# Optimization experiments

Hardware: AMD Instinct MI355X
Metric: run time of the kernel (lower is better)

The kernel has to match this reference:

```python
import jax, jax.numpy as jnp
import numpy as np

N_NODES = 50000
N_EDGES = 800000
IN_CH = 128
OUT_CH = 64
HEADS = 8


def setup_inputs() -> dict:
    key = jax.random.key(0)
    k1, k2, k3, k4 = jax.random.split(key, 4)
    x = jax.random.normal(k1, (N_NODES, IN_CH), dtype=jnp.float32)
    edge_index = jax.random.randint(k2, (2, N_EDGES), 0, N_NODES, dtype=jnp.int32)
    # xavier-uniform-ish scale
    W = jax.random.normal(k3, (IN_CH, OUT_CH), dtype=jnp.float32) * (1.0 / np.sqrt(IN_CH))
    attn_weights = jax.random.normal(k4, (2 * OUT_CH, 1), dtype=jnp.float32) * (1.0 / np.sqrt(2 * OUT_CH))
    return {"x": x, "edge_index": edge_index, "W": W, "attn_weights": attn_weights}


def reference(x, edge_index, W, attn_weights):
    # h: [N, out]
    h = x @ W
    ei, ej = edge_index[0], edge_index[1]
    h_i = h[ei]                      # [E, out] gather by destination
    h_j = h[ej]                      # [E, out] gather by source
    edge_feat = jnp.concatenate([h_i, h_j], axis=-1)  # [E, 2*out]
    logits = jax.nn.leaky_relu(edge_feat @ attn_weights, negative_slope=0.2)  # [E, 1]
    # NOTE: original does softmax over dim=0 -> GLOBAL softmax over all edges
    alpha = jax.nn.softmax(logits, axis=0)  # [E, 1]
    # dropout p=0.6 is a no-op in eval mode (training=False)
    msg = h_j * alpha                # [E, out]
    h_head = jnp.zeros_like(h).at[ei].add(msg)  # scatter-add into destinations
    # All heads share W and attn_weights (see source loop), so with dropout off
    # every head is identical; concat == tile along feature dim.
    return jnp.tile(h_head, (1, HEADS))  # [N, out*heads]
```

## Files before the change

kernel.cpp:

```cpp
#include <hip/hip_runtime.h>

#define N_NODES 50000
#define N_EDGES 800000
#define IN_CH 128
#define OUT_CH 64
#define HEADS 8
#define ROW 512
#define NBLK_G 782
#define NBLK_A 782
#define NBIN 196
#define BINCAP 4608
#define MAXDEG 64
#define WS_STRIDE 136

typedef float f4 __attribute__((ext_vector_type(4)));
typedef short bf16x8 __attribute__((ext_vector_type(8)));

__device__ __forceinline__ float lrelu(float z) {
    return z > 0.0f ? z : 0.2f * z;
}

__device__ __forceinline__ unsigned f2b(float f) {
    unsigned u = __float_as_uint(f);
    return (u + 0x7FFFu + ((u >> 16) & 1u)) >> 16;
}

__global__ __launch_bounds__(256) void gemm_bin(const float* __restrict__ x,
                                                const float* __restrict__ W,
                                                const float* __restrict__ attn,
                                                const int4* __restrict__ ei4,
                                                const int4* __restrict__ ej4,
                                                unsigned short* __restrict__ hbuf,
                                                float* __restrict__ s,
                                                float* __restrict__ t,
                                                int* __restrict__ bin_count,
                                                unsigned* __restrict__ binned) {
    __shared__ unsigned short xs[64 * WS_STRIDE];
    __shared__ unsigned short wls[64 * WS_STRIDE];
    const int tid = threadIdx.x;
    const int bid = blockIdx.x;

    if (bid & 1) {
        unsigned* hist = (unsigned*)xs;
        unsigned* bse  = hist + NBIN;
        unsigned* cur  = bse + NBIN;
        if (tid < NBIN) { hist[tid] = 0u; cur[tid] = 0u; }
        __syncthreads();
        const int g = (bid >> 1) * 256 + tid;
        const bool act = g < N_EDGES / 4;
        int4 li = make_int4(0, 0, 0, 0), lj = make_int4(0, 0, 0, 0);
        if (act) {
            li = ei4[g];
            lj = ej4[g];
            atomicAdd(&hist[li.x >> 8], 1u);
            atomicAdd(&hist[li.y >> 8], 1u);
            atomicAdd(&hist[li.z >> 8], 1u);
            atomicAdd(&hist[li.w >> 8], 1u);
        }
        __syncthreads();
        if (tid < NBIN) {
            const unsigned c = hist[tid];
            bse[tid] = c ? (unsigned)atomicAdd(&bin_count[tid], (int)c) : 0u;
        }
        __syncthreads();
        if (act) {
            const unsigned p0 = bse[li.x >> 8] + atomicAdd(&cur[li.x >> 8], 1u);
            if (p0 < BINCAP) binned[(li.x >> 8) * BINCAP + p0] =
                ((unsigned)(li.x & 255) << 16) | (unsigned)lj.x;
            const unsigned p1 = bse[li.y >> 8] + atomicAdd(&cur[li.y >> 8], 1u);
            if (p1 < BINCAP) binned[(li.y >> 8) * BINCAP + p1] =
                ((unsigned)(li.y & 255) << 16) | (unsigned)lj.y;
            const unsigned p2 = bse[li.z >> 8] + atomicAdd(&cur[li.z >> 8], 1u);
            if (p2 < BINCAP) binned[(li.z >> 8) * BINCAP + p2] =
                ((unsigned)(li.z & 255) << 16) | (unsigned)lj.z;
            const unsigned p3 = bse[li.w >> 8] + atomicAdd(&cur[li.w >> 8], 1u);
            if (p3 < BINCAP) binned[(li.w >> 8) * BINCAP + p3] =
                ((unsigned)(li.w & 255) << 16) | (unsigned)lj.w;
        }
        return;
    }

    const int base = (bid >> 1) * 64;
    {
        const float4* W4 = (const float4*)W;
#pragma unroll
        for (int j = 0; j < 8; ++j) {
            const int idx = tid + j * 256;
            const int k = idx >> 4;
            const int c = (idx & 15) * 4;
            const float4 v = W4[idx];
            wls[(c + 0) * WS_STRIDE + k] = (unsigned short)f2b(v.x);
            wls[(c + 1) * WS_STRIDE + k] = (unsigned short)f2b(v.y);
            wls[(c + 2) * WS_STRIDE + k] = (unsigned short)f2b(v.z);
            wls[(c + 3) * WS_STRIDE + k] = (unsigned short)f2b(v.w);
        }
    }
    {
        const float4* x4 = (const float4*)x;
#pragma unroll
        for (int j = 0; j < 8; ++j) {
            const int idx = tid + j * 256;
            const int r = idx >> 5;
            const int kq = idx & 31;
            const int row = base + r;
            float4 v = make_float4(0.f, 0.f, 0.f, 0.f);
            if (row < N_NODES) v = x4[row * 32 + kq];
            ushort4 pb;
            pb.x = (unsigned short)f2b(v.x);
            pb.y = (unsigned short)f2b(v.y);
            pb.z = (unsigned short)f2b(v.z);
            pb.w = (unsigned short)f2b(v.w);
            *(ushort4*)&xs[r * WS_STRIDE + kq * 4] = pb;
        }
    }
    __syncthreads();
    const int w = tid >> 6, lane = tid & 63;
    const int m = lane & 15;
    const int kq = lane >> 4;
    bf16x8 afr[4];
#pragma unroll
    for (int kb = 0; kb < 4; ++kb)
        afr[kb] = *(const bf16x8*)&xs[(w * 16 + m) * WS_STRIDE + kb * 32 + kq * 8];
    float sacc[4] = {0.f, 0.f, 0.f, 0.f};
    float tacc[4] = {0.f, 0.f, 0.f, 0.f};
#pragma unroll
    for (int ct = 0; ct < 4; ++ct) {
        f4 acc = {0.f, 0.f, 0.f, 0.f};
#pragma unroll
        for (int kb = 0; kb < 4; ++kb) {
            const bf16x8 b = *(const bf16x8*)&wls[(ct * 16 + m) * WS_STRIDE + kb * 32 + kq * 8];
            acc = __builtin_amdgcn_mfma_f32_16x16x32_bf16(afr[kb], b, acc, 0, 0, 0);
        }
        const float a1 = attn[ct * 16 + m];
        const float a2 = attn[64 + ct * 16 + m];
#pragma unroll
        for (int r = 0; r < 4; ++r) {
            sacc[r] = fmaf(acc[r], a1, sacc[r]);
            tacc[r] = fmaf(acc[r], a2, tacc[r]);
            const int row = base + w * 16 + kq * 4 + r;
            if (row < N_NODES)
                hbuf[row * OUT_CH + ct * 16 + m] = (unsigned short)f2b(acc[r]);
        }
    }
#pragma unroll
    for (int off = 1; off < 16; off <<= 1) {
#pragma unroll
        for (int r = 0; r < 4; ++r) {
            sacc[r] += __shfl_xor(sacc[r], off, 64);
            tacc[r] += __shfl_xor(tacc[r], off, 64);
        }
    }
    if (m == 0) {
#pragma unroll
        for (int r = 0; r < 4; ++r) {
            const int row = base + w * 16 + kq * 4 + r;
            if (row < N_NODES) { s[row] = sacc[r]; t[row] = tacc[r]; }
        }
    }
}

__global__ __launch_bounds__(1024) void weight_pass(const unsigned* __restrict__ binned,
                                                    const int* __restrict__ bin_count,
                                                    const float* __restrict__ s,
                                                    const float* __restrict__ t,
                                                    unsigned* __restrict__ cv,
                                                    int* __restrict__ count,
                                                    float* __restrict__ Zsum) {
    __shared__ unsigned bkt[256 * MAXDEG];
    __shared__ unsigned cnt_l[256];
    __shared__ float s_l[256];
    __shared__ float red[16];
    const int tid = threadIdx.x;
    const int bin = blockIdx.x;
    if (tid < 256) {
        cnt_l[tid] = 0u;
        const int d = bin * 256 + tid;
        s_l[tid] = (d < N_NODES) ? s[d] : 0.0f;
    }
    __syncthreads();
    int n = bin_count[bin];
    if (n > BINCAP) n = BINCAP;
    float zs = 0.0f;
    for (int i = tid; i < n; i += 1024) {
        const unsigned e = binned[bin * BINCAP + i];
        const int dl = (int)((e >> 16) & 255u);
        const int src = (int)(e & 0xFFFFu);
        const float w = __expf(lrelu(s_l[dl] + t[src]));
        zs += w;
        const unsigned r = atomicAdd(&cnt_l[dl], 1u);
        if (r < MAXDEG) bkt[dl * MAXDEG + r] = (f2b(w) << 16) | (unsigned)src;
    }
    __syncthreads();
    {
        uint4* cv4 = (uint4*)(cv + bin * (256 * MAXDEG));
        const uint4* b4 = (const uint4*)bkt;
        for (int i = tid; i < 4096; i += 1024) cv4[i] = b4[i];
    }
    if (tid < 256) {
        const int d = bin * 256 + tid;
        if (d < N_NODES) count[d] = (int)cnt_l[tid];
    }
#pragma unroll
    for (int off = 32; off > 0; off >>= 1)
        zs += __shfl_down(zs, off, 64);
    if ((tid & 63) == 0) red[tid >> 6] = zs;
    __syncthreads();
    if (tid == 0) {
        float v = 0.0f;
#pragma unroll
        for (int k = 0; k < 16; ++k) v += red[k];
        atomicAdd(Zsum, v);
    }
}

__global__ __launch_bounds__(256) void gather_out(const int* __restrict__ count,
                                                  const unsigned* __restrict__ cv,
                                                  const float* __restrict__ Zsum,
                                                  const unsigned short* __restrict__ hbuf,
                                                  float* __restrict__ out) {
    const int n = blockIdx.x * 4 + (threadIdx.x >> 6);
    const int lane = threadIdx.x & 63;
    const int slot = lane >> 3;
    const int q = lane & 7;
    const float z = 1.0f / Zsum[0];
    int cnt = count[n];
    cnt = cnt < MAXDEG ? cnt : MAXDEG;
    const int base = n * MAXDEG;
    const uint4* h4 = (const uint4*)hbuf;
    f4 a0 = (f4)(0.0f);
    f4 a1 = (f4)(0.0f);
    unsigned pk = 0u;
    if (slot < cnt) pk = cv[base + slot];
    for (int i = 0; i < cnt; i += 8) {
        const int c = (int)(pk & 0xFFFFu);
        const float w = __uint_as_float(pk & 0xFFFF0000u);
        unsigned pk_n = 0u;
        const int ee = i + 8 + slot;
        if (ee < cnt) pk_n = cv[base + ee];
        const uint4 hv = h4[c * 8 + q];
        a0.x = fmaf(w, __uint_as_float(hv.x << 16),        a0.x);
        a0.y = fmaf(w, __uint_as_float(hv.x & 0xFFFF0000u), a0.y);
        a0.z = fmaf(w, __uint_as_float(hv.y << 16),        a0.z);
        a0.w = fmaf(w, __uint_as_float(hv.y & 0xFFFF0000u), a0.w);
        a1.x = fmaf(w, __uint_as_float(hv.z << 16),        a1.x);
        a1.y = fmaf(w, __uint_as_float(hv.z & 0xFFFF0000u), a1.y);
        a1.z = fmaf(w, __uint_as_float(hv.w << 16),        a1.z);
        a1.w = fmaf(w, __uint_as_float(hv.w & 0xFFFF0000u), a1.w);
        pk = pk_n;
    }
#pragma unroll
    for (int off = 8; off <= 32; off <<= 1) {
        a0.x += __shfl_xor(a0.x, off, 64);
        a0.y += __shfl_xor(a0.y, off, 64);
        a0.z += __shfl_xor(a0.z, off, 64);
        a0.w += __shfl_xor(a0.w, off, 64);
        a1.x += __shfl_xor(a1.x, off, 64);
        a1.y += __shfl_xor(a1.y, off, 64);
        a1.z += __shfl_xor(a1.z, off, 64);
        a1.w += __shfl_xor(a1.w, off, 64);
    }
    a0 *= z;
    a1 *= z;
    f4* out4 = (f4*)out;
    const int ob = n * 128 + slot * 16 + q * 2;
    __builtin_nontemporal_store(a0, out4 + ob);
    __builtin_nontemporal_store(a1, out4 + ob + 1);
}

extern "C" void kernel_launch(void* const* d_in, const int* in_sizes, int n_in,
                              void* d_out, int out_size, void* d_ws, size_t ws_size,
                              hipStream_t stream) {
    const float* x    = (const float*)d_in[0];
    const int*   eidx = (const int*)d_in[1];
    const float* W    = (const float*)d_in[2];
    const float* attn = (const float*)d_in[3];
    float* out = (float*)d_out;

    unsigned short* hbuf = (unsigned short*)d_ws;
    unsigned* cv    = (unsigned*)(hbuf + N_NODES * OUT_CH);
    float* s        = (float*)(cv + NBIN * 256 * MAXDEG);
    float* t        = s + N_NODES;
    int* bin_count  = (int*)(t + N_NODES);
    float* Zsum     = (float*)(bin_count + NBIN);
    unsigned* binned= (unsigned*)(Zsum + 1);
    int* count      = (int*)(binned + NBIN * BINCAP);

    const int4* ei4 = (const int4*)eidx;
    const int4* ej4 = (const int4*)(eidx + N_EDGES);

    hipMemsetAsync(bin_count, 0, (NBIN + 1) * sizeof(int), stream);
    gemm_bin   <<<NBLK_G + NBLK_A, 256, 0, stream>>>(x, W, attn, ei4, ej4,
                                                     hbuf, s, t, bin_count, binned);
    weight_pass<<<NBIN, 1024, 0, stream>>>(binned, bin_count, s, t, cv, count, Zsum);
    gather_out <<<N_NODES / 4, 256, 0, stream>>>(count, cv, Zsum, hbuf, out);
}
```

Measured before the change: 173.8 us.

## Fuse weight pass and gather into one cooperative kernel with grid sync

Merges the weight computation and the per-node gather into a single cooperative kernel. The per-destination buckets stay in shared memory, so the cv/count round trip through global memory and one kernel launch go away. A grid-wide sync waits for the global softmax denominator before the gather runs. In exchange the gather now runs on only 196 blocks of 1024 threads, one per bin, which lowers parallelism and may leave the GPU underused. The 64KB shared bucket array also limits occupancy.

```diff
diff --git a/kernel.cpp b/kernel.cpp
--- a/kernel.cpp
+++ b/kernel.cpp
@@ -1,4 +1,7 @@
 #include <hip/hip_runtime.h>
+#include <hip/hip_cooperative_groups.h>
+
+namespace cg = cooperative_groups;
 
 #define N_NODES 50000
 #define N_EDGES 800000
@@ -159,17 +162,19 @@
     }
 }
 
-__global__ __launch_bounds__(1024) void weight_pass(const unsigned* __restrict__ binned,
-                                                    const int* __restrict__ bin_count,
-                                                    const float* __restrict__ s,
-                                                    const float* __restrict__ t,
-                                                    unsigned* __restrict__ cv,
-                                                    int* __restrict__ count,
-                                                    float* __restrict__ Zsum) {
+__global__ __launch_bounds__(1024) void weight_gather(
+        const unsigned* __restrict__ binned,
+        const int* __restrict__ bin_count,
+        const float* __restrict__ s,
+        const float* __restrict__ t,
+        const unsigned short* __restrict__ hbuf,
+        float* __restrict__ Zsum,
+        float* __restrict__ out) {
     __shared__ unsigned bkt[256 * MAXDEG];
     __shared__ unsigned cnt_l[256];
     __shared__ float s_l[256];
     __shared__ float red[16];
+    __shared__ float zsh;
     const int tid = threadIdx.x;
     const int bin = blockIdx.x;
     if (tid < 256) {
@@ -190,16 +195,6 @@
         const unsigned r = atomicAdd(&cnt_l[dl], 1u);
         if (r < MAXDEG) bkt[dl * MAXDEG + r] = (f2b(w) << 16) | (unsigned)src;
     }
-    __syncthreads();
-    {
-        uint4* cv4 = (uint4*)(cv + bin * (256 * MAXDEG));
-        const uint4* b4 = (const uint4*)bkt;
-        for (int i = tid; i < 4096; i += 1024) cv4[i] = b4[i];
-    }
-    if (tid < 256) {
-        const int d = bin * 256 + tid;
-        if (d < N_NODES) count[d] = (int)cnt_l[tid];
-    }
 #pragma unroll
     for (int off = 32; off > 0; off >>= 1)
         zs += __shfl_down(zs, off, 64);
@@ -211,60 +206,57 @@
         for (int k = 0; k < 16; ++k) v += red[k];
         atomicAdd(Zsum, v);
     }
-}
-
-__global__ __launch_bounds__(256) void gather_out(const int* __restrict__ count,
-                                                  const unsigned* __restrict__ cv,
-                                                  const float* __restrict__ Zsum,
-                                                  const unsigned short* __restrict__ hbuf,
-                                                  float* __restrict__ out) {
-    const int n = blockIdx.x * 4 + (threadIdx.x >> 6);
-    const int lane = threadIdx.x & 63;
+    __threadfence();
+    cg::this_grid().sync();
+    if (tid == 0) zsh = 1.0f / *(volatile float*)Zsum;
+    __syncthreads();
+    const float z = zsh;
+    const int wv = tid >> 6, lane = tid & 63;
     const int slot = lane >> 3;
     const int q = lane & 7;
-    const float z = 1.0f / Zsum[0];
-    int cnt = count[n];
-    cnt = cnt < MAXDEG ? cnt : MAXDEG;
-    const int base = n * MAXDEG;
     const uint4* h4 = (const uint4*)hbuf;
-    f4 a0 = (f4)(0.0f);
-    f4 a1 = (f4)(0.0f);
-    unsigned pk = 0u;
-    if (slot < cnt) pk = cv[base + slot];
-    for (int i = 0; i < cnt; i += 8) {
-        const int c = (int)(pk & 0xFFFFu);
-        const float w = __uint_as_float(pk & 0xFFFF0000u);
-        unsigned pk_n = 0u;
-        const int ee = i + 8 + slot;
-        if (ee < cnt) pk_n = cv[base + ee];
-        const uint4 hv = h4[c * 8 + q];
-        a0.x = fmaf(w, __uint_as_float(hv.x << 16),        a0.x);
-        a0.y = fmaf(w, __uint_as_float(hv.x & 0xFFFF0000u), a0.y);
-        a0.z = fmaf(w, __uint_as_float(hv.y << 16),        a0.z);
-        a0.w = fmaf(w, __uint_as_float(hv.y & 0xFFFF0000u), a0.w);
-        a1.x = fmaf(w, __uint_as_float(hv.z << 16),        a1.x);
-        a1.y = fmaf(w, __uint_as_float(hv.z & 0xFFFF0000u), a1.y);
-        a1.z = fmaf(w, __uint_as_float(hv.w << 16),        a1.z);
-        a1.w = fmaf(w, __uint_as_float(hv.w & 0xFFFF0000u), a1.w);
-        pk = pk_n;
-    }
-#pragma unroll
-    for (int off = 8; off <= 32; off <<= 1) {
-        a0.x += __shfl_xor(a0.x, off, 64);
-        a0.y += __shfl_xor(a0.y, off, 64);
-        a0.z += __shfl_xor(a0.z, off, 64);
-        a0.w += __shfl_xor(a0.w, off, 64);
-        a1.x += __shfl_xor(a1.x, off, 64);
-        a1.y += __shfl_xor(a1.y, off, 64);
-        a1.z += __shfl_xor(a1.z, off, 64);
-        a1.w += __shfl_xor(a1.w, off, 64);
-    }
-    a0 *= z;
-    a1 *= z;
     f4* out4 = (f4*)out;
-    const int ob = n * 128 + slot * 16 + q * 2;
-    __builtin_nontemporal_store(a0, out4 + ob);
-    __builtin_nontemporal_store(a1, out4 + ob + 1);
+    for (int k = 0; k < 16; ++k) {
+        const int dl = wv * 16 + k;
+        const int node = bin * 256 + dl;
+        if (node >= N_NODES) break;
+        int cnt = (int)cnt_l[dl];
+        cnt = cnt < MAXDEG ? cnt : MAXDEG;
+        f4 a0 = (f4)(0.0f);
+        f4 a1 = (f4)(0.0f);
+        for (int i = 0; i < cnt; i += 8) {
+            const int ee = i + slot;
+            unsigned pk = 0u;
+            if (ee < cnt) pk = bkt[dl * MAXDEG + ee];
+            const int c = (int)(pk & 0xFFFFu);
+            const float w = __uint_as_float(pk & 0xFFFF0000u);
+            const uint4 hv = h4[c * 8 + q];
+            a0.x = fmaf(w, __uint_as_float(hv.x << 16),        a0.x);
+            a0.y = fmaf(w, __uint_as_float(hv.x & 0xFFFF0000u), a0.y);
+            a0.z = fmaf(w, __uint_as_float(hv.y << 16),        a0.z);
+            a0.w = fmaf(w, __uint_as_float(hv.y & 0xFFFF0000u), a0.w);
+            a1.x = fmaf(w, __uint_as_float(hv.z << 16),        a1.x);
+            a1.y = fmaf(w, __uint_as_float(hv.z & 0xFFFF0000u), a1.y);
+            a1.z = fmaf(w, __uint_as_float(hv.w << 16),        a1.z);
+            a1.w = fmaf(w, __uint_as_float(hv.w & 0xFFFF0000u), a1.w);
+        }
+#pragma unroll
+        for (int off = 8; off <= 32; off <<= 1) {
+            a0.x += __shfl_xor(a0.x, off, 64);
+            a0.y += __shfl_xor(a0.y, off, 64);
+            a0.z += __shfl_xor(a0.z, off, 64);
+            a0.w += __shfl_xor(a0.w, off, 64);
+            a1.x += __shfl_xor(a1.x, off, 64);
+            a1.y += __shfl_xor(a1.y, off, 64);
+            a1.z += __shfl_xor(a1.z, off, 64);
+            a1.w += __shfl_xor(a1.w, off, 64);
+        }
+        a0 *= z;
+        a1 *= z;
+        const int ob = node * 128 + slot * 16 + q * 2;
+        __builtin_nontemporal_store(a0, out4 + ob);
+        __builtin_nontemporal_store(a1, out4 + ob + 1);
+    }
 }
 
 extern "C" void kernel_launch(void* const* d_in, const int* in_sizes, int n_in,
@@ -277,20 +269,29 @@
     float* out = (float*)d_out;
 
     unsigned short* hbuf = (unsigned short*)d_ws;
-    unsigned* cv    = (unsigned*)(hbuf + N_NODES * OUT_CH);
-    float* s        = (float*)(cv + NBIN * 256 * MAXDEG);
+    float* s        = (float*)(hbuf + N_NODES * OUT_CH);
     float* t        = s + N_NODES;
     int* bin_count  = (int*)(t + N_NODES);
     float* Zsum     = (float*)(bin_count + NBIN);
     unsigned* binned= (unsigned*)(Zsum + 1);
-    int* count      = (int*)(binned + NBIN * BINCAP);
 
     const int4* ei4 = (const int4*)eidx;
     const int4* ej4 = (const int4*)(eidx + N_EDGES);
 
     hipMemsetAsync(bin_count, 0, (NBIN + 1) * sizeof(int), stream);
-    gemm_bin   <<<NBLK_G + NBLK_A, 256, 0, stream>>>(x, W, attn, ei4, ej4,
-                                                     hbuf, s, t, bin_count, binned);
-    weight_pass<<<NBIN, 1024, 0, stream>>>(binned, bin_count, s, t, cv, count, Zsum);
-    gather_out <<<N_NODES / 4, 256, 0, stream>>>(count, cv, Zsum, hbuf, out);
-}
+    gemm_bin<<<NBLK_G + NBLK_A, 256, 0, stream>>>(x, W, attn, ei4, ej4,
+                                                  hbuf, s, t, bin_count, binned);
+    {
+        const unsigned* a_binned   = binned;
+        const int*      a_bincnt   = bin_count;
+        const float*    a_s        = s;
+        const float*    a_t        = t;
+        const unsigned short* a_h  = hbuf;
+        float*          a_Z        = Zsum;
+        float*          a_out      = out;
+        void* args[] = {(void*)&a_binned, (void*)&a_bincnt, (void*)&a_s,
+                        (void*)&a_t, (void*)&a_h, (void*)&a_Z, (void*)&a_out};
+        hipLaunchCooperativeKernel((const void*)weight_gather, dim3(NBIN),
+                                   dim3(1024), args, 0, stream);
+    }
+}
```

Result: slower. 267.8 us (+54.1%).

## Replace global bin atomics with per-cell fixed-capacity bin slots

Applied to the files above, without the earlier changes.

The binning blocks now write each edge into a per-(bin, cell) slot of capacity 32 using only shared-memory atomics, and record per-cell counts. This removes the global atomicAdd on bin_count and the extra histogram pass and barrier. weight_pass then walks 782 cells per bin with uint4 loads. In exchange the scan is irregular, with one thread per cell doing serial work. Edges are dropped if a cell overflows 32 entries, though the expected count per cell is about 5.

```diff
diff --git a/kernel.cpp b/kernel.cpp
--- a/kernel.cpp
+++ b/kernel.cpp
@@ -8,8 +8,9 @@
 #define ROW 512
 #define NBLK_G 782
 #define NBLK_A 782
+#define NCELL NBLK_A
 #define NBIN 196
-#define BINCAP 4608
+#define CAP2 32
 #define MAXDEG 64
 #define WS_STRIDE 136
 
@@ -33,7 +34,7 @@
                                                 unsigned short* __restrict__ hbuf,
                                                 float* __restrict__ s,
                                                 float* __restrict__ t,
-                                                int* __restrict__ bin_count,
+                                                unsigned* __restrict__ cellcnt,
                                                 unsigned* __restrict__ binned) {
     __shared__ unsigned short xs[64 * WS_STRIDE];
     __shared__ unsigned short wls[64 * WS_STRIDE];
@@ -41,41 +42,32 @@
     const int bid = blockIdx.x;
 
     if (bid & 1) {
-        unsigned* hist = (unsigned*)xs;
-        unsigned* bse  = hist + NBIN;
-        unsigned* cur  = bse + NBIN;
-        if (tid < NBIN) { hist[tid] = 0u; cur[tid] = 0u; }
+        unsigned* cur = (unsigned*)xs;
+        if (tid < NBIN) cur[tid] = 0u;
         __syncthreads();
-        const int g = (bid >> 1) * 256 + tid;
-        const bool act = g < N_EDGES / 4;
-        int4 li = make_int4(0, 0, 0, 0), lj = make_int4(0, 0, 0, 0);
-        if (act) {
-            li = ei4[g];
-            lj = ej4[g];
-            atomicAdd(&hist[li.x >> 8], 1u);
-            atomicAdd(&hist[li.y >> 8], 1u);
-            atomicAdd(&hist[li.z >> 8], 1u);
-            atomicAdd(&hist[li.w >> 8], 1u);
+        const int cell = bid >> 1;
+        const int g = cell * 256 + tid;
+        if (g < N_EDGES / 4) {
+            const int4 li = ei4[g];
+            const int4 lj = ej4[g];
+            const int b0 = li.x >> 8, b1 = li.y >> 8, b2 = li.z >> 8, b3 = li.w >> 8;
+            const unsigned p0 = atomicAdd(&cur[b0], 1u);
+            if (p0 < CAP2) binned[(unsigned)(b0 * NCELL + cell) * CAP2 + p0] =
+                ((unsigned)(li.x & 255) << 16) | (unsigned)lj.x;
+            const unsigned p1 = atomicAdd(&cur[b1], 1u);
+            if (p1 < CAP2) binned[(unsigned)(b1 * NCELL + cell) * CAP2 + p1] =
+                ((unsigned)(li.y & 255) << 16) | (unsigned)lj.y;
+            const unsigned p2 = atomicAdd(&cur[b2], 1u);
+            if (p2 < CAP2) binned[(unsigned)(b2 * NCELL + cell) * CAP2 + p2] =
+                ((unsigned)(li.z & 255) << 16) | (unsigned)lj.z;
+            const unsigned p3 = atomicAdd(&cur[b3], 1u);
+            if (p3 < CAP2) binned[(unsigned)(b3 * NCELL + cell) * CAP2 + p3] =
+                ((unsigned)(li.w & 255) << 16) | (unsigned)lj.w;
         }
         __syncthreads();
         if (tid < NBIN) {
-            const unsigned c = hist[tid];
-            bse[tid] = c ? (unsigned)atomicAdd(&bin_count[tid], (int)c) : 0u;
-        }
-        __syncthreads();
-        if (act) {
-            const unsigned p0 = bse[li.x >> 8] + atomicAdd(&cur[li.x >> 8], 1u);
-            if (p0 < BINCAP) binned[(li.x >> 8) * BINCAP + p0] =
-                ((unsigned)(li.x & 255) << 16) | (unsigned)lj.x;
-            const unsigned p1 = bse[li.y >> 8] + atomicAdd(&cur[li.y >> 8], 1u);
-            if (p1 < BINCAP) binned[(li.y >> 8) * BINCAP + p1] =
-                ((unsigned)(li.y & 255) << 16) | (unsigned)lj.y;
-            const unsigned p2 = bse[li.z >> 8] + atomicAdd(&cur[li.z >> 8], 1u);
-            if (p2 < BINCAP) binned[(li.z >> 8) * BINCAP + p2] =
-                ((unsigned)(li.z & 255) << 16) | (unsigned)lj.z;
-            const unsigned p3 = bse[li.w >> 8] + atomicAdd(&cur[li.w >> 8], 1u);
-            if (p3 < BINCAP) binned[(li.w >> 8) * BINCAP + p3] =
-                ((unsigned)(li.w & 255) << 16) | (unsigned)lj.w;
+            const unsigned c = cur[tid];
+            cellcnt[(unsigned)tid * NCELL + cell] = c < CAP2 ? c : CAP2;
         }
         return;
     }
@@ -160,7 +152,7 @@
 }
 
 __global__ __launch_bounds__(1024) void weight_pass(const unsigned* __restrict__ binned,
-                                                    const int* __restrict__ bin_count,
+                                                    const unsigned* __restrict__ cellcnt,
                                                     const float* __restrict__ s,
                                                     const float* __restrict__ t,
                                                     unsigned* __restrict__ cv,
@@ -178,18 +170,29 @@
         s_l[tid] = (d < N_NODES) ? s[d] : 0.0f;
     }
     __syncthreads();
-    int n = bin_count[bin];
-    if (n > BINCAP) n = BINCAP;
     float zs = 0.0f;
-    for (int i = tid; i < n; i += 1024) {
-        const unsigned e = binned[bin * BINCAP + i];
-        const int dl = (int)((e >> 16) & 255u);
-        const int src = (int)(e & 0xFFFFu);
-        const float w = __expf(lrelu(s_l[dl] + t[src]));
-        zs += w;
-        const unsigned r = atomicAdd(&cnt_l[dl], 1u);
-        if (r < MAXDEG) bkt[dl * MAXDEG + r] = (f2b(w) << 16) | (unsigned)src;
-    }
+#define PROC(eu) do { \
+        const unsigned e = (eu); \
+        const int dl = (int)((e >> 16) & 255u); \
+        const int src = (int)(e & 0xFFFFu); \
+        const float wv_ = __expf(lrelu(s_l[dl] + t[src])); \
+        zs += wv_; \
+        const unsigned r_ = atomicAdd(&cnt_l[dl], 1u); \
+        if (r_ < MAXDEG) bkt[dl * MAXDEG + r_] = (f2b(wv_) << 16) | (unsigned)src; \
+    } while (0)
+    for (int c = tid; c < NCELL; c += 1024) {
+        const int cnt = (int)cellcnt[(unsigned)bin * NCELL + c];
+        const uint4* cp4 = (const uint4*)&binned[(unsigned)(bin * NCELL + c) * CAP2];
+        for (int k4 = 0; k4 * 4 < cnt; ++k4) {
+            const uint4 e4 = cp4[k4];
+            const int kb = k4 * 4;
+            PROC(e4.x);
+            if (kb + 1 < cnt) PROC(e4.y);
+            if (kb + 2 < cnt) PROC(e4.z);
+            if (kb + 3 < cnt) PROC(e4.w);
+        }
+    }
+#undef PROC
     __syncthreads();
     {
         uint4* cv4 = (uint4*)(cv + bin * (256 * MAXDEG));
@@ -277,20 +280,20 @@
     float* out = (float*)d_out;
 
     unsigned short* hbuf = (unsigned short*)d_ws;
-    unsigned* cv    = (unsigned*)(hbuf + N_NODES * OUT_CH);
-    float* s        = (float*)(cv + NBIN * 256 * MAXDEG);
-    float* t        = s + N_NODES;
-    int* bin_count  = (int*)(t + N_NODES);
-    float* Zsum     = (float*)(bin_count + NBIN);
-    unsigned* binned= (unsigned*)(Zsum + 1);
-    int* count      = (int*)(binned + NBIN * BINCAP);
+    unsigned* binned = (unsigned*)(hbuf + N_NODES * OUT_CH);
+    unsigned* cv     = binned + NBIN * NCELL * CAP2;
+    float* s         = (float*)(cv + NBIN * 256 * MAXDEG);
+    float* t         = s + N_NODES;
+    int* count       = (int*)(t + N_NODES);
+    unsigned* cellcnt= (unsigned*)(count + N_NODES);
+    float* Zsum      = (float*)(cellcnt + NBIN * NCELL);
 
     const int4* ei4 = (const int4*)eidx;
     const int4* ej4 = (const int4*)(eidx + N_EDGES);
 
-    hipMemsetAsync(bin_count, 0, (NBIN + 1) * sizeof(int), stream);
+    hipMemsetAsync(Zsum, 0, sizeof(float), stream);
     gemm_bin   <<<NBLK_G + NBLK_A, 256, 0, stream>>>(x, W, attn, ei4, ej4,
-                                                     hbuf, s, t, bin_count, binned);
-    weight_pass<<<NBIN, 1024, 0, stream>>>(binned, bin_count, s, t, cv, count, Zsum);
+                                                     hbuf, s, t, cellcnt, binned);
+    weight_pass<<<NBIN, 1024, 0, stream>>>(binned, cellcnt, s, t, cv, count, Zsum);
     gather_out <<<N_NODES / 4, 256, 0, stream>>>(count, cv, Zsum, hbuf, out);
 }
```

Measured after the change: 178.3 us. 1.03x slower.
